# Optimization experiments

Measured on AMD Instinct MI355X. Metric: run time of the kernel, lower is better.

Reference implementation:

```python
import jax, jax.numpy as jnp
import numpy as np

WEIGHT = 0.5  # PenalizeLoss(weight=0.5)
B, C = 1048576, 128


def setup_inputs() -> dict:
    key = jax.random.key(0)
    k1, k2 = jax.random.split(key)
    predicts = jax.random.normal(k1, (B, C), dtype=jnp.float32)
    targets = jax.random.randint(k2, (B,), 0, C, dtype=jnp.int64)
    return {"predicts": predicts, "targets": targets}


def reference(predicts, targets):
    # softmax probabilities (original: torch.softmax(predicts, dim=1))
    p = jax.nn.softmax(predicts, axis=1)  # [B, C]
    # CE: mean over batch of -log(p[i, target_i]) == -log(sum(p * one_hot))
    log_p = jax.nn.log_softmax(predicts, axis=1)
    ce_loss = -jnp.mean(jnp.take_along_axis(log_p, targets[:, None], axis=1))
    # penalty: samples where true class == 1 but argmax prediction == 0
    predictions = jnp.argmax(p, axis=1)  # [B]
    mask = (targets == 1) & (predictions == 0)  # [B] bool
    count = jnp.sum(mask)
    p0 = p[:, 0]
    # log(1 / (1 - p0)) = -log1p(-p0); mask inputs first to keep values finite
    p0_safe = jnp.where(mask, p0, 0.0)
    pen_sum = jnp.sum(-jnp.log1p(-p0_safe))
    penalty_loss = jnp.where(count > 0, pen_sum / count.astype(p.dtype), 0.0)
    return ce_loss + WEIGHT * penalty_loss
```

## Files before the change

### kernel.cpp

```cpp
#include <hip/hip_runtime.h>
#include <math.h>

#define CLS 128
#define PEN_WEIGHT 0.5f
#define ROWS_PER_BLOCK 256

__global__ __launch_bounds__(256) void penalize_loss_main(
        const float* __restrict__ predicts,
        const int*   __restrict__ targets,
        float* __restrict__ ws, int B, int nb) {
    const int tid  = threadIdx.x;
    const int lane = tid & 63;
    const int wave = tid >> 6;
    const int gl   = lane & 15;

    float acc_ce = 0.0f, acc_pen = 0.0f, acc_cnt = 0.0f;

    const int r_block = blockIdx.x * ROWS_PER_BLOCK;
    for (int i = 0; i < 16; ++i) {
        const int r = r_block + i * 16 + wave * 4 + (lane >> 4);
        if (r < B) {
            const float* row = predicts + (size_t)r * CLS;
            const float4 v1 = *(const float4*)(row + gl * 4);
            const float4 v2 = *(const float4*)(row + 64 + gl * 4);
            const int t = targets[r];

            float lm = fmaxf(fmaxf(fmaxf(v1.x, v1.y), fmaxf(v1.z, v1.w)),
                             fmaxf(fmaxf(v2.x, v2.y), fmaxf(v2.z, v2.w)));
            lm = fmaxf(lm, __shfl_xor(lm, 1, 64));
            lm = fmaxf(lm, __shfl_xor(lm, 2, 64));
            lm = fmaxf(lm, __shfl_xor(lm, 4, 64));
            lm = fmaxf(lm, __shfl_xor(lm, 8, 64));

            float e = __expf(v1.x - lm) + __expf(v1.y - lm)
                    + __expf(v1.z - lm) + __expf(v1.w - lm)
                    + __expf(v2.x - lm) + __expf(v2.y - lm)
                    + __expf(v2.z - lm) + __expf(v2.w - lm);
            e += __shfl_xor(e, 1, 64);
            e += __shfl_xor(e, 2, 64);
            e += __shfl_xor(e, 4, 64);
            e += __shfl_xor(e, 8, 64);

            const unsigned long long b = __ballot(v1.x == lm);
            const bool pred0 = (b >> (lane & 48)) & 1ull;

            if (gl == 0) {
                acc_ce += lm + __logf(e);
                if (t == 1 && pred0) {
                    acc_pen += -log1pf(-1.0f / e);
                    acc_cnt += 1.0f;
                }
            }
            if (gl == ((t >> 2) & 15)) {
                const int j = t & 3;
                float xt;
                if (t & 64) xt = (j == 0) ? v2.x : (j == 1) ? v2.y : (j == 2) ? v2.z : v2.w;
                else        xt = (j == 0) ? v1.x : (j == 1) ? v1.y : (j == 2) ? v1.z : v1.w;
                acc_ce -= xt;
            }
        }
    }

    for (int mask = 1; mask < 64; mask <<= 1) {
        acc_ce  += __shfl_xor(acc_ce,  mask, 64);
        acc_pen += __shfl_xor(acc_pen, mask, 64);
        acc_cnt += __shfl_xor(acc_cnt, mask, 64);
    }

    __shared__ float s_ce[4], s_pen[4], s_cnt[4];
    if (lane == 0) { s_ce[wave] = acc_ce; s_pen[wave] = acc_pen; s_cnt[wave] = acc_cnt; }
    __syncthreads();
    if (tid == 0) {
        ws[blockIdx.x]          = s_ce[0]  + s_ce[1]  + s_ce[2]  + s_ce[3];
        ws[nb + blockIdx.x]     = s_pen[0] + s_pen[1] + s_pen[2] + s_pen[3];
        ws[2 * nb + blockIdx.x] = s_cnt[0] + s_cnt[1] + s_cnt[2] + s_cnt[3];
    }
}

__global__ __launch_bounds__(256) void finalize_kernel(
        const float* __restrict__ ws, float* __restrict__ out, int B, int nb) {
    const int tid  = threadIdx.x;
    const int lane = tid & 63;
    const int wave = tid >> 6;

    float ce = 0.0f, pen = 0.0f, cnt = 0.0f;
    for (int i = tid; i < nb; i += 256) {
        ce  += ws[i];
        pen += ws[nb + i];
        cnt += ws[2 * nb + i];
    }
    for (int mask = 1; mask < 64; mask <<= 1) {
        ce  += __shfl_xor(ce,  mask, 64);
        pen += __shfl_xor(pen, mask, 64);
        cnt += __shfl_xor(cnt, mask, 64);
    }
    __shared__ float s_ce[4], s_pen[4], s_cnt[4];
    if (lane == 0) { s_ce[wave] = ce; s_pen[wave] = pen; s_cnt[wave] = cnt; }
    __syncthreads();
    if (tid == 0) {
        const float tce  = s_ce[0]  + s_ce[1]  + s_ce[2]  + s_ce[3];
        const float tpen = s_pen[0] + s_pen[1] + s_pen[2] + s_pen[3];
        const float tcnt = s_cnt[0] + s_cnt[1] + s_cnt[2] + s_cnt[3];
        const float mean_ce  = tce / (float)B;
        const float mean_pen = (tcnt > 0.0f) ? (tpen / tcnt) : 0.0f;
        out[0] = mean_ce + PEN_WEIGHT * mean_pen;
    }
}

extern "C" void kernel_launch(void* const* d_in, const int* in_sizes, int n_in,
                              void* d_out, int out_size, void* d_ws, size_t ws_size,
                              hipStream_t stream) {
    const float* predicts = (const float*)d_in[0];
    const int*   targets  = (const int*)d_in[1];
    const int B = in_sizes[1];
    float* ws  = (float*)d_ws;
    float* out = (float*)d_out;

    const int nb = (B + ROWS_PER_BLOCK - 1) / ROWS_PER_BLOCK;
    penalize_loss_main<<<nb, 256, 0, stream>>>(predicts, targets, ws, B, nb);
    finalize_kernel<<<1, 256, 0, stream>>>(ws, out, B, nb);
}
```

Baseline: 684.8 us.

## Software-pipeline row loads three deep with nontemporal loads and drop ballot

The per-block row loop becomes a manual three-stage software pipeline: loads for later row groups are issued before computing the current one, and they use nontemporal vector loads. Full blocks take this pipelined path and partial tail blocks keep the old guarded loop. The ballot-based argmax-is-class-0 check is replaced by a direct comparison in the lane that owns class 0. The aim is to keep more memory requests in flight on a bandwidth-bound streaming reduction, at the cost of extra registers and redundant clamped reloads of the last row group.

```diff
diff --git a/kernel.cpp b/kernel.cpp
--- a/kernel.cpp
+++ b/kernel.cpp
@@ -4,6 +4,9 @@
 #define CLS 128
 #define PEN_WEIGHT 0.5f
 #define ROWS_PER_BLOCK 256
+#define NIT 16
+
+typedef float v4f __attribute__((ext_vector_type(4)));
 
 __global__ __launch_bounds__(256) void penalize_loss_main(
         const float* __restrict__ predicts,
@@ -13,50 +16,90 @@
     const int lane = tid & 63;
     const int wave = tid >> 6;
     const int gl   = lane & 15;
+    const int sub  = lane >> 4;
 
     float acc_ce = 0.0f, acc_pen = 0.0f, acc_cnt = 0.0f;
 
     const int r_block = blockIdx.x * ROWS_PER_BLOCK;
-    for (int i = 0; i < 16; ++i) {
-        const int r = r_block + i * 16 + wave * 4 + (lane >> 4);
-        if (r < B) {
-            const float* row = predicts + (size_t)r * CLS;
-            const float4 v1 = *(const float4*)(row + gl * 4);
-            const float4 v2 = *(const float4*)(row + 64 + gl * 4);
-            const int t = targets[r];
+    const int r0 = r_block + wave * 4 + sub;
 
-            float lm = fmaxf(fmaxf(fmaxf(v1.x, v1.y), fmaxf(v1.z, v1.w)),
-                             fmaxf(fmaxf(v2.x, v2.y), fmaxf(v2.z, v2.w)));
-            lm = fmaxf(lm, __shfl_xor(lm, 1, 64));
-            lm = fmaxf(lm, __shfl_xor(lm, 2, 64));
-            lm = fmaxf(lm, __shfl_xor(lm, 4, 64));
-            lm = fmaxf(lm, __shfl_xor(lm, 8, 64));
+    auto compute = [&](const v4f v1, const v4f v2, const int t) {
+        float lm = fmaxf(fmaxf(fmaxf(v1.x, v1.y), fmaxf(v1.z, v1.w)),
+                         fmaxf(fmaxf(v2.x, v2.y), fmaxf(v2.z, v2.w)));
+        lm = fmaxf(lm, __shfl_xor(lm, 1, 64));
+        lm = fmaxf(lm, __shfl_xor(lm, 2, 64));
+        lm = fmaxf(lm, __shfl_xor(lm, 4, 64));
+        lm = fmaxf(lm, __shfl_xor(lm, 8, 64));
 
-            float e = __expf(v1.x - lm) + __expf(v1.y - lm)
-                    + __expf(v1.z - lm) + __expf(v1.w - lm)
-                    + __expf(v2.x - lm) + __expf(v2.y - lm)
-                    + __expf(v2.z - lm) + __expf(v2.w - lm);
-            e += __shfl_xor(e, 1, 64);
-            e += __shfl_xor(e, 2, 64);
-            e += __shfl_xor(e, 4, 64);
-            e += __shfl_xor(e, 8, 64);
+        float e = __expf(v1.x - lm) + __expf(v1.y - lm)
+                + __expf(v1.z - lm) + __expf(v1.w - lm)
+                + __expf(v2.x - lm) + __expf(v2.y - lm)
+                + __expf(v2.z - lm) + __expf(v2.w - lm);
+        e += __shfl_xor(e, 1, 64);
+        e += __shfl_xor(e, 2, 64);
+        e += __shfl_xor(e, 4, 64);
+        e += __shfl_xor(e, 8, 64);
 
-            const unsigned long long b = __ballot(v1.x == lm);
-            const bool pred0 = (b >> (lane & 48)) & 1ull;
+        if (gl == 0) {
+            acc_ce += lm + __logf(e);
+            if (t == 1 && v1.x == lm) {
+                acc_pen += -log1pf(-1.0f / e);
+                acc_cnt += 1.0f;
+            }
+        }
+        if (gl == ((t >> 2) & 15)) {
+            const int j = t & 3;
+            float xt;
+            if (t & 64) xt = (j == 0) ? v2.x : (j == 1) ? v2.y : (j == 2) ? v2.z : v2.w;
+            else        xt = (j == 0) ? v1.x : (j == 1) ? v1.y : (j == 2) ? v1.z : v1.w;
+            acc_ce -= xt;
+        }
+    };
 
-            if (gl == 0) {
-                acc_ce += lm + __logf(e);
-                if (t == 1 && pred0) {
-                    acc_pen += -log1pf(-1.0f / e);
-                    acc_cnt += 1.0f;
-                }
-            }
-            if (gl == ((t >> 2) & 15)) {
-                const int j = t & 3;
-                float xt;
-                if (t & 64) xt = (j == 0) ? v2.x : (j == 1) ? v2.y : (j == 2) ? v2.z : v2.w;
-                else        xt = (j == 0) ? v1.x : (j == 1) ? v1.y : (j == 2) ? v1.z : v1.w;
-                acc_ce -= xt;
+    if (r_block + ROWS_PER_BLOCK <= B) {
+        const float* base = predicts + (size_t)r0 * CLS + gl * 4;
+
+#define LOADRG(V1, V2, T, idx) do {                                   \
+            const float* _p = base + (size_t)(idx) * (16 * CLS);      \
+            V1 = __builtin_nontemporal_load((const v4f*)_p);          \
+            V2 = __builtin_nontemporal_load((const v4f*)(_p + 64));   \
+            T  = targets[r0 + (idx) * 16];                            \
+        } while (0)
+
+        v4f A1, A2, B1, B2, C1, C2;
+        int At, Bt, Ct;
+        LOADRG(A1, A2, At, 0);
+        LOADRG(B1, B2, Bt, 1);
+        LOADRG(C1, C2, Ct, 2);
+
+        #pragma unroll 1
+        for (int i = 0; i < NIT - 1; i += 3) {
+            const int pa = (i + 3 < NIT) ? i + 3 : NIT - 1;
+            const int pb = (i + 4 < NIT) ? i + 4 : NIT - 1;
+            const int pc = (i + 5 < NIT) ? i + 5 : NIT - 1;
+
+            v4f t1 = A1, t2 = A2; int tt = At;
+            LOADRG(A1, A2, At, pa);
+            compute(t1, t2, tt);
+
+            t1 = B1; t2 = B2; tt = Bt;
+            LOADRG(B1, B2, Bt, pb);
+            compute(t1, t2, tt);
+
+            t1 = C1; t2 = C2; tt = Ct;
+            LOADRG(C1, C2, Ct, pc);
+            compute(t1, t2, tt);
+        }
+        compute(A1, A2, At);
+#undef LOADRG
+    } else {
+        for (int i = 0; i < NIT; ++i) {
+            const int r = r0 + i * 16;
+            if (r < B) {
+                const float* row = predicts + (size_t)r * CLS;
+                const v4f v1 = *(const v4f*)(row + gl * 4);
+                const v4f v2 = *(const v4f*)(row + 64 + gl * 4);
+                compute(v1, v2, targets[r]);
             }
         }
     }
```

After: 653.3 us. 1.05x faster.
